# Kernel tuning notes

Measured on AMD Instinct MI355X. Metric: run time of the kernel, lower is better.

The kernel has to match this reference:

```python
import jax, jax.numpy as jnp
import numpy as np

D_K = 64  # key dim -> temperature = sqrt(64) = 8.0


def setup_inputs() -> dict:
    key = jax.random.key(0)
    k1, k2, k3, k4 = jax.random.split(key, 4)
    N, P, d_k, d_v = 4, 4096, 64, 256
    k_src = jax.random.normal(k1, (N, P, d_k), dtype=jnp.float32)
    v_src = jax.random.normal(k2, (N, P, d_v), dtype=jnp.float32)
    q_tgr = jax.random.normal(k3, (N, P, d_k), dtype=jnp.float32)
    # 1x1 conv (d_v -> d_v) == per-position linear; kaiming-style init
    W_fc = jax.random.normal(k4, (d_v, d_v), dtype=jnp.float32) * (1.0 / np.sqrt(d_v))
    b_fc = jnp.zeros((d_v,), dtype=jnp.float32)
    return {"k_src": k_src, "v_src": v_src, "q_tgr": q_tgr, "W_fc": W_fc, "b_fc": b_fc}


def reference(k_src, v_src, q_tgr, W_fc, b_fc):
    temperature = jnp.asarray(np.sqrt(D_K), dtype=q_tgr.dtype)
    # scaled dot-product attention: [N,P,P] scores (mask=None, dropout=eval/identity)
    attn = jnp.einsum("npd,nqd->npq", q_tgr, k_src) / temperature
    attn = jax.nn.softmax(attn, axis=2)
    out = jnp.einsum("npq,nqc->npc", attn, v_src)  # [N,P,d_v]
    # fc: 1x1 conv over (N*P, C, 1, 1) == linear over channel dim
    out = jnp.einsum("npc,oc->npo", out, W_fc) + b_fc
    return out
```

## Files before the change

### kernel.cpp

```cpp
#include <hip/hip_runtime.h>
#include <hip/hip_bf16.h>

#define NB 4
#define PSEQ 4096
#define DK 64
#define DV 256

typedef __attribute__((ext_vector_type(8))) short short8;
typedef __attribute__((ext_vector_type(16))) float f32x16;
typedef __attribute__((ext_vector_type(4))) unsigned int uint4v;

__device__ __forceinline__ float bf2f(unsigned short u) {
    union { unsigned int i; float f; } v; v.i = ((unsigned int)u) << 16; return v.f;
}
__device__ __forceinline__ unsigned short f2bf(float f) {
    union { float f; unsigned int i; } v; v.f = f;
    return (unsigned short)((v.i + 0x7fffu + ((v.i >> 16) & 1u)) >> 16);
}

__device__ __forceinline__ short8 gload16(const void* p) {
    short8 r;
    asm volatile("global_load_dwordx4 %0, %1, off"
                 : "=v"(r) : "v"(p) : "memory");
    return r;
}

__global__ __launch_bounds__(256) void prep_all(
    const float* __restrict__ q, const float* __restrict__ k,
    const float* __restrict__ wfc, const float* __restrict__ v,
    unsigned short* __restrict__ Qh, unsigned short* __restrict__ Ql,
    unsigned short* __restrict__ Kp,
    unsigned short* __restrict__ Wb, unsigned short* __restrict__ Vp) {
    __shared__ float tile[64][65];
    const int b = blockIdx.x, tid = threadIdx.x;
    if (b < 1024) {
        const int i = (b * 256 + tid) * 4;
        float4 x = *reinterpret_cast<const float4*>(q + i);
        ushort4 h, l;
        h.x = f2bf(x.x); l.x = f2bf(x.x - bf2f(h.x));
        h.y = f2bf(x.y); l.y = f2bf(x.y - bf2f(h.y));
        h.z = f2bf(x.z); l.z = f2bf(x.z - bf2f(h.z));
        h.w = f2bf(x.w); l.w = f2bf(x.w - bf2f(h.w));
        *reinterpret_cast<ushort4*>(Qh + i) = h;
        *reinterpret_cast<ushort4*>(Ql + i) = l;
    } else if (b < 1536) {
        const int idx = b - 1024;
        const int n = idx >> 7, g = idx & 127;
        const int d = tid >> 6, lane = tid & 63;
        const int l31 = lane & 31, hi = lane >> 5;
        const float* src = k + ((size_t)(n * PSEQ + g * 32 + l31)) * DK + d * 16 + hi * 8;
        float x[8];
        *reinterpret_cast<float4*>(&x[0]) = *reinterpret_cast<const float4*>(src);
        *reinterpret_cast<float4*>(&x[4]) = *reinterpret_cast<const float4*>(src + 4);
        short8 o;
#pragma unroll
        for (int j = 0; j < 8; ++j) o[j] = (short)f2bf(x[j]);
        *reinterpret_cast<short8*>(
            Kp + (((size_t)n * 512 + g * 4 + d) * 64 + lane) * 8) = o;
    } else if (b < 1600) {
        const int i = ((b - 1536) * 256 + tid) * 4;
        float4 x = *reinterpret_cast<const float4*>(wfc + i);
        ushort4 h;
        h.x = f2bf(x.x); h.y = f2bf(x.y); h.z = f2bf(x.z); h.w = f2bf(x.w);
        *reinterpret_cast<ushort4*>(Wb + i) = h;
    } else {
        const int vtid = b - 1600;
        const int k0 = (vtid & 63) * 64, c0 = ((vtid >> 6) & 3) * 64, n = vtid >> 8;
        const int gb = (vtid & 63) * 2;
        const int cb = ((vtid >> 6) & 3) * 2;
        const float* vn = v + (size_t)n * PSEQ * DV;
        const int tx = tid & 15, ty = tid >> 4;
#pragma unroll
        for (int rep = 0; rep < 4; ++rep) {
            int r = ty + rep * 16;
            float4 d = *reinterpret_cast<const float4*>(vn + (size_t)(k0 + r) * DV + c0 + tx * 4);
            tile[r][tx * 4 + 0] = d.x; tile[r][tx * 4 + 1] = d.y;
            tile[r][tx * 4 + 2] = d.z; tile[r][tx * 4 + 3] = d.w;
        }
        __syncthreads();
#pragma unroll
        for (int uu = 0; uu < 2; ++uu) {
            const int u = tid * 2 + uu;
            const int lane = u & 63;
            const int slot = (u >> 6) & 1;
            const int c32l = (u >> 7) & 1;
            const int gl   = (u >> 8) & 1;
            const int l31 = lane & 31, hi = lane >> 5;
            const int keyl = gl * 32 + slot * 16 + hi * 8;
            const int chl = c32l * 32 + l31;
            short8 o;
#pragma unroll
            for (int j = 0; j < 8; ++j) o[j] = (short)f2bf(tile[keyl + j][chl]);
            *reinterpret_cast<short8*>(
                Vp + ((((size_t)n * 128 + gb + gl) * 8 + cb + c32l) * 2 + slot) * 512
                   + lane * 8) = o;
        }
    }
}

__global__ __launch_bounds__(256, 2) void attn_wave(
    const unsigned short* __restrict__ Kp,
    const unsigned short* __restrict__ Qh,
    const unsigned short* __restrict__ Ql,
    const unsigned short* __restrict__ Vp,
    const unsigned short* __restrict__ Wg,
    const float* __restrict__ Bg,
    float* __restrict__ Og)
{
    __shared__ float Of32[32][128];
    __shared__ unsigned short Omrg[32][132];
    __shared__ float Lsh[32];

    const int tid = threadIdx.x;
    const int w = tid >> 6;
    const int lane = tid & 63;
    const int l31 = lane & 31;
    const int hi = lane >> 5;

    const int id = blockIdx.x;
    const int n   = (id & 7) >> 1;
    const int chb = id & 1;
    const int q0  = (id >> 3) * 32;

    if (tid < 32) Lsh[tid] = 0.f;
    __syncthreads();

    const unsigned short* Kpn = Kp + (size_t)n * 512 * 512;
    const unsigned short* Vpn = Vp + (size_t)n * 128 * 8 * 2 * 512;

    short8 qhf[4], qlf[4];
#pragma unroll
    for (int d = 0; d < 4; ++d) {
        const size_t a = ((size_t)n * PSEQ + q0 + l31) * DK + d * 16 + hi * 8;
        qhf[d] = *reinterpret_cast<const short8*>(Qh + a);
        qlf[d] = *reinterpret_cast<const short8*>(Ql + a);
    }

    const f32x16 Z16 = {0.f,0.f,0.f,0.f, 0.f,0.f,0.f,0.f,
                        0.f,0.f,0.f,0.f, 0.f,0.f,0.f,0.f};
    f32x16 oacc[4];
#pragma unroll
    for (int ct = 0; ct < 4; ++ct) oacc[ct] = Z16;

    float lsum = 0.f;
    const float SC = 0.125f * 1.44269504088896340736f;

    short8 vv[8];

    auto issueK = [&](int kt, short8 (&kf)[4]) {
        const int g = w * 32 + (kt < 31 ? kt : 31);
#pragma unroll
        for (int d = 0; d < 4; ++d)
            kf[d] = gload16(Kpn + ((size_t)(g * 4 + d) * 64 + lane) * 8);
    };
    auto issueV = [&](int kt) {
        const int g = w * 32 + (kt < 31 ? kt : 31);
#pragma unroll
        for (int ct = 0; ct < 4; ++ct) {
            const size_t vb = (((size_t)g * 8 + chb * 4 + ct) * 2) * 512;
            vv[ct]     = gload16(Vpn + vb + lane * 8);
            vv[4 + ct] = gload16(Vpn + vb + 512 + lane * 8);
        }
    };

    auto TILE = [&](int kt, short8 (&kfC)[4]) {
        f32x16 s = Z16;
        __builtin_amdgcn_s_setprio(1);
#pragma unroll
        for (int d = 0; d < 4; ++d)
            s = __builtin_amdgcn_mfma_f32_32x32x16_bf16(kfC[d], qhf[d], s, 0, 0, 0);
#pragma unroll
        for (int d = 0; d < 4; ++d)
            s = __builtin_amdgcn_mfma_f32_32x32x16_bf16(kfC[d], qlf[d], s, 0, 0, 0);
        __builtin_amdgcn_s_setprio(0);

        issueK(kt + 2, kfC);

        unsigned int pk[8];
        float lacc = 0.f;
#pragma unroll
        for (int j = 0; j < 8; ++j) {
            float p0 = exp2f(s[2 * j] * SC);
            float p1 = exp2f(s[2 * j + 1] * SC);
            lacc += p0 + p1;
            asm("v_cvt_pk_bf16_f32 %0, %1, %2" : "=v"(pk[j]) : "v"(p0), "v"(p1));
        }
        lsum += lacc;
        asm volatile("v_permlane32_swap_b32 %0, %1" : "+v"(pk[0]), "+v"(pk[2]));
        asm volatile("v_permlane32_swap_b32 %0, %1" : "+v"(pk[1]), "+v"(pk[3]));
        asm volatile("v_permlane32_swap_b32 %0, %1" : "+v"(pk[4]), "+v"(pk[6]));
        asm volatile("v_permlane32_swap_b32 %0, %1" : "+v"(pk[5]), "+v"(pk[7]));
        union { uint4v u; short8 s8; } cvt0, cvt1;
        cvt0.u = (uint4v){pk[0], pk[1], pk[2], pk[3]};
        cvt1.u = (uint4v){pk[4], pk[5], pk[6], pk[7]};
        const short8 pa0 = cvt0.s8, pa1 = cvt1.s8;

        asm volatile("s_waitcnt vmcnt(4)" ::: "memory");
        __builtin_amdgcn_sched_barrier(0);

        __builtin_amdgcn_s_setprio(1);
#pragma unroll
        for (int ct = 0; ct < 4; ++ct)
            oacc[ct] = __builtin_amdgcn_mfma_f32_32x32x16_bf16(pa0, vv[ct], oacc[ct], 0, 0, 0);
#pragma unroll
        for (int ct = 0; ct < 4; ++ct)
            oacc[ct] = __builtin_amdgcn_mfma_f32_32x32x16_bf16(pa1, vv[4 + ct], oacc[ct], 0, 0, 0);
        __builtin_amdgcn_s_setprio(0);

        issueV(kt + 1);
    };

    short8 kfA[4], kfB[4];
    issueK(0, kfA);
    issueK(1, kfB);
    issueV(0);
    asm volatile("s_waitcnt vmcnt(12)" ::: "memory");
    __builtin_amdgcn_sched_barrier(0);

#pragma unroll 1
    for (int kt = 0; kt < 32; kt += 2) {
        TILE(kt, kfA);
        TILE(kt + 1, kfB);
    }
    asm volatile("s_waitcnt vmcnt(0)" ::: "memory");

    lsum += __shfl_xor(lsum, 32, 64);
    if (lane < 32) atomicAdd(&Lsh[l31], lsum);

    if (w == 0) {
#pragma unroll
        for (int ct = 0; ct < 4; ++ct)
#pragma unroll
            for (int r = 0; r < 16; ++r) {
                const int row = (r & 3) + 8 * (r >> 2) + 4 * hi;
                Of32[row][ct * 32 + l31] = oacc[ct][r];
            }
    }
    __syncthreads();
    if (w == 1) {
#pragma unroll
        for (int ct = 0; ct < 4; ++ct)
#pragma unroll
            for (int r = 0; r < 16; ++r) {
                const int row = (r & 3) + 8 * (r >> 2) + 4 * hi;
                Of32[row][ct * 32 + l31] += oacc[ct][r];
            }
    }
    __syncthreads();
    if (w == 2) {
#pragma unroll
        for (int ct = 0; ct < 4; ++ct)
#pragma unroll
            for (int r = 0; r < 16; ++r) {
                const int row = (r & 3) + 8 * (r >> 2) + 4 * hi;
                Of32[row][ct * 32 + l31] += oacc[ct][r];
            }
    }
    __syncthreads();
    if (w == 3) {
#pragma unroll
        for (int ct = 0; ct < 4; ++ct)
#pragma unroll
            for (int r = 0; r < 16; ++r) {
                const int row = (r & 3) + 8 * (r >> 2) + 4 * hi;
                Of32[row][ct * 32 + l31] += oacc[ct][r];
            }
    }
    __syncthreads();

    {
        const int row = tid >> 3;
        const int col0 = (tid & 7) * 16;
        const float il = 1.0f / Lsh[row];
#pragma unroll
        for (int j = 0; j < 4; ++j) {
            float4 xv = *reinterpret_cast<const float4*>(&Of32[row][col0 + j * 4]);
            ushort4 o;
            o.x = f2bf(xv.x * il); o.y = f2bf(xv.y * il);
            o.z = f2bf(xv.z * il); o.w = f2bf(xv.w * il);
            *reinterpret_cast<ushort4*>(&Omrg[row][col0 + j * 4]) = o;
        }
    }
    __syncthreads();

    f32x16 fa0 = Z16, fa1 = Z16;
#pragma unroll
    for (int slot = 0; slot < 8; ++slot) {
        short8 af = *reinterpret_cast<const short8*>(&Omrg[l31][slot * 16 + hi * 8]);
        short8 w0 = *reinterpret_cast<const short8*>(
            Wg + (size_t)(w * 64 + l31) * DV + chb * 128 + slot * 16 + hi * 8);
        short8 w1 = *reinterpret_cast<const short8*>(
            Wg + (size_t)(w * 64 + 32 + l31) * DV + chb * 128 + slot * 16 + hi * 8);
        fa0 = __builtin_amdgcn_mfma_f32_32x32x16_bf16(af, w0, fa0, 0, 0, 0);
        fa1 = __builtin_amdgcn_mfma_f32_32x32x16_bf16(af, w1, fa1, 0, 0, 0);
    }
    {
        const float b0 = chb == 0 ? Bg[w * 64 + l31] : 0.f;
        const float b1 = chb == 0 ? Bg[w * 64 + 32 + l31] : 0.f;
#pragma unroll
        for (int r = 0; r < 16; ++r) {
            const int row = (r & 3) + 8 * (r >> 2) + 4 * hi;
            const size_t orow = ((size_t)n * PSEQ + q0 + row) * DV;
            atomicAdd(&Og[orow + w * 64 + l31],      fa0[r] + b0);
            atomicAdd(&Og[orow + w * 64 + 32 + l31], fa1[r] + b1);
        }
    }
}

extern "C" void kernel_launch(void* const* d_in, const int* in_sizes, int n_in,
                              void* d_out, int out_size, void* d_ws, size_t ws_size,
                              hipStream_t stream) {
    const float* k_src = (const float*)d_in[0];
    const float* v_src = (const float*)d_in[1];
    const float* q_tgr = (const float*)d_in[2];
    const float* W_fc  = (const float*)d_in[3];
    const float* b_fc  = (const float*)d_in[4];
    float* out = (float*)d_out;

    char* wsb = (char*)d_ws;
    unsigned short* Vp = (unsigned short*)(wsb);
    unsigned short* Qh = (unsigned short*)(wsb + 8388608);
    unsigned short* Ql = (unsigned short*)(wsb + 10485760);
    unsigned short* Kp = (unsigned short*)(wsb + 12582912);
    unsigned short* Wb = (unsigned short*)(wsb + 14680064);

    prep_all<<<2624, 256, 0, stream>>>(q_tgr, k_src, W_fc, v_src,
                                       Qh, Ql, Kp, Wb, Vp);
    hipMemsetAsync(d_out, 0, (size_t)out_size, stream);
    attn_wave<<<1024, 256, 0, stream>>>(Kp, Qh, Ql, Vp, Wb, b_fc, out);
}
```

Measured before the change: 188.9 us.

## Process 64 query rows per block with 8 waves sharing K/V tiles

Doubles the block to 512 threads so two groups of four waves handle 64 query rows while walking the same key/value partition, halving the grid. Because the K/V slices line up across query groups, the second group's global loads can hit in cache. This cuts K/V traffic per query. The fc epilogue is reorganised so each wave loads one 32-column W slice into registers and reuses it across two row tiles. The cost is larger shared memory, a bigger block with possible register-pressure limits at launch bounds (512,2), and fewer blocks to balance across CUs.

```diff
diff --git a/kernel.cpp b/kernel.cpp
--- a/kernel.cpp
+++ b/kernel.cpp
@@ -98,7 +98,7 @@
     }
 }
 
-__global__ __launch_bounds__(256, 2) void attn_wave(
+__global__ __launch_bounds__(512, 2) void attn_wave(
     const unsigned short* __restrict__ Kp,
     const unsigned short* __restrict__ Qh,
     const unsigned short* __restrict__ Ql,
@@ -107,12 +107,14 @@
     const float* __restrict__ Bg,
     float* __restrict__ Og)
 {
-    __shared__ float Of32[32][128];
-    __shared__ unsigned short Omrg[32][132];
-    __shared__ float Lsh[32];
+    __shared__ float Of32[64][128];
+    __shared__ unsigned short Omrg[64][132];
+    __shared__ float Lsh[64];
 
     const int tid = threadIdx.x;
     const int w = tid >> 6;
+    const int kq = w & 3;
+    const int qh = w >> 2;
     const int lane = tid & 63;
     const int l31 = lane & 31;
     const int hi = lane >> 5;
@@ -120,9 +122,9 @@
     const int id = blockIdx.x;
     const int n   = (id & 7) >> 1;
     const int chb = id & 1;
-    const int q0  = (id >> 3) * 32;
-
-    if (tid < 32) Lsh[tid] = 0.f;
+    const int q0  = (id >> 3) * 64;
+
+    if (tid < 64) Lsh[tid] = 0.f;
     __syncthreads();
 
     const unsigned short* Kpn = Kp + (size_t)n * 512 * 512;
@@ -131,7 +133,7 @@
     short8 qhf[4], qlf[4];
 #pragma unroll
     for (int d = 0; d < 4; ++d) {
-        const size_t a = ((size_t)n * PSEQ + q0 + l31) * DK + d * 16 + hi * 8;
+        const size_t a = ((size_t)n * PSEQ + q0 + qh * 32 + l31) * DK + d * 16 + hi * 8;
         qhf[d] = *reinterpret_cast<const short8*>(Qh + a);
         qlf[d] = *reinterpret_cast<const short8*>(Ql + a);
     }
@@ -148,13 +150,13 @@
     short8 vv[8];
 
     auto issueK = [&](int kt, short8 (&kf)[4]) {
-        const int g = w * 32 + (kt < 31 ? kt : 31);
+        const int g = kq * 32 + (kt < 31 ? kt : 31);
 #pragma unroll
         for (int d = 0; d < 4; ++d)
             kf[d] = gload16(Kpn + ((size_t)(g * 4 + d) * 64 + lane) * 8);
     };
     auto issueV = [&](int kt) {
-        const int g = w * 32 + (kt < 31 ? kt : 31);
+        const int g = kq * 32 + (kt < 31 ? kt : 31);
 #pragma unroll
         for (int ct = 0; ct < 4; ++ct) {
             const size_t vb = (((size_t)g * 8 + chb * 4 + ct) * 2) * 512;
@@ -225,44 +227,44 @@
     asm volatile("s_waitcnt vmcnt(0)" ::: "memory");
 
     lsum += __shfl_xor(lsum, 32, 64);
-    if (lane < 32) atomicAdd(&Lsh[l31], lsum);
-
-    if (w == 0) {
-#pragma unroll
-        for (int ct = 0; ct < 4; ++ct)
-#pragma unroll
-            for (int r = 0; r < 16; ++r) {
-                const int row = (r & 3) + 8 * (r >> 2) + 4 * hi;
+    if (lane < 32) atomicAdd(&Lsh[qh * 32 + l31], lsum);
+
+    if (kq == 0) {
+#pragma unroll
+        for (int ct = 0; ct < 4; ++ct)
+#pragma unroll
+            for (int r = 0; r < 16; ++r) {
+                const int row = qh * 32 + (r & 3) + 8 * (r >> 2) + 4 * hi;
                 Of32[row][ct * 32 + l31] = oacc[ct][r];
             }
     }
     __syncthreads();
-    if (w == 1) {
-#pragma unroll
-        for (int ct = 0; ct < 4; ++ct)
-#pragma unroll
-            for (int r = 0; r < 16; ++r) {
-                const int row = (r & 3) + 8 * (r >> 2) + 4 * hi;
+    if (kq == 1) {
+#pragma unroll
+        for (int ct = 0; ct < 4; ++ct)
+#pragma unroll
+            for (int r = 0; r < 16; ++r) {
+                const int row = qh * 32 + (r & 3) + 8 * (r >> 2) + 4 * hi;
                 Of32[row][ct * 32 + l31] += oacc[ct][r];
             }
     }
     __syncthreads();
-    if (w == 2) {
-#pragma unroll
-        for (int ct = 0; ct < 4; ++ct)
-#pragma unroll
-            for (int r = 0; r < 16; ++r) {
-                const int row = (r & 3) + 8 * (r >> 2) + 4 * hi;
+    if (kq == 2) {
+#pragma unroll
+        for (int ct = 0; ct < 4; ++ct)
+#pragma unroll
+            for (int r = 0; r < 16; ++r) {
+                const int row = qh * 32 + (r & 3) + 8 * (r >> 2) + 4 * hi;
                 Of32[row][ct * 32 + l31] += oacc[ct][r];
             }
     }
     __syncthreads();
-    if (w == 3) {
-#pragma unroll
-        for (int ct = 0; ct < 4; ++ct)
-#pragma unroll
-            for (int r = 0; r < 16; ++r) {
-                const int row = (r & 3) + 8 * (r >> 2) + 4 * hi;
+    if (kq == 3) {
+#pragma unroll
+        for (int ct = 0; ct < 4; ++ct)
+#pragma unroll
+            for (int r = 0; r < 16; ++r) {
+                const int row = qh * 32 + (r & 3) + 8 * (r >> 2) + 4 * hi;
                 Of32[row][ct * 32 + l31] += oacc[ct][r];
             }
     }
@@ -283,27 +285,32 @@
     }
     __syncthreads();
 
-    f32x16 fa0 = Z16, fa1 = Z16;
-#pragma unroll
-    for (int slot = 0; slot < 8; ++slot) {
-        short8 af = *reinterpret_cast<const short8*>(&Omrg[l31][slot * 16 + hi * 8]);
-        short8 w0 = *reinterpret_cast<const short8*>(
-            Wg + (size_t)(w * 64 + l31) * DV + chb * 128 + slot * 16 + hi * 8);
-        short8 w1 = *reinterpret_cast<const short8*>(
-            Wg + (size_t)(w * 64 + 32 + l31) * DV + chb * 128 + slot * 16 + hi * 8);
-        fa0 = __builtin_amdgcn_mfma_f32_32x32x16_bf16(af, w0, fa0, 0, 0, 0);
-        fa1 = __builtin_amdgcn_mfma_f32_32x32x16_bf16(af, w1, fa1, 0, 0, 0);
+    f32x16 fa[2];
+    fa[0] = Z16; fa[1] = Z16;
+    short8 wf[8];
+#pragma unroll
+    for (int slot = 0; slot < 8; ++slot)
+        wf[slot] = *reinterpret_cast<const short8*>(
+            Wg + (size_t)(w * 32 + l31) * DV + chb * 128 + slot * 16 + hi * 8);
+#pragma unroll
+    for (int rt = 0; rt < 2; ++rt) {
+#pragma unroll
+        for (int slot = 0; slot < 8; ++slot) {
+            short8 af = *reinterpret_cast<const short8*>(
+                &Omrg[rt * 32 + l31][slot * 16 + hi * 8]);
+            fa[rt] = __builtin_amdgcn_mfma_f32_32x32x16_bf16(af, wf[slot], fa[rt], 0, 0, 0);
+        }
     }
     {
-        const float b0 = chb == 0 ? Bg[w * 64 + l31] : 0.f;
-        const float b1 = chb == 0 ? Bg[w * 64 + 32 + l31] : 0.f;
-#pragma unroll
-        for (int r = 0; r < 16; ++r) {
-            const int row = (r & 3) + 8 * (r >> 2) + 4 * hi;
-            const size_t orow = ((size_t)n * PSEQ + q0 + row) * DV;
-            atomicAdd(&Og[orow + w * 64 + l31],      fa0[r] + b0);
-            atomicAdd(&Og[orow + w * 64 + 32 + l31], fa1[r] + b1);
-        }
+        const float b0 = chb == 0 ? Bg[w * 32 + l31] : 0.f;
+#pragma unroll
+        for (int rt = 0; rt < 2; ++rt)
+#pragma unroll
+            for (int r = 0; r < 16; ++r) {
+                const int row = rt * 32 + (r & 3) + 8 * (r >> 2) + 4 * hi;
+                const size_t orow = ((size_t)n * PSEQ + q0 + row) * DV;
+                atomicAdd(&Og[orow + w * 32 + l31], fa[rt][r] + b0);
+            }
     }
 }
 
@@ -327,5 +334,5 @@
     prep_all<<<2624, 256, 0, stream>>>(q_tgr, k_src, W_fc, v_src,
                                        Qh, Ql, Kp, Wb, Vp);
     hipMemsetAsync(d_out, 0, (size_t)out_size, stream);
-    attn_wave<<<1024, 256, 0, stream>>>(Kp, Qh, Ql, Vp, Wb, b_fc, out);
-}
+    attn_wave<<<512, 512, 0, stream>>>(Kp, Qh, Ql, Vp, Wb, b_fc, out);
+}
```

After: 199.6 us. 5.6% more time.
